# Kernel optimization log

Measured on AMD Instinct MI355X. Metric: run time of the kernel, lower is better.

Reference implementation:

```python
import jax, jax.numpy as jnp
import numpy as np

POS_INF = 64500.0
B, P, C = 32, 2048, 256
D = C // 2


def setup_inputs() -> dict:
    key = jax.random.key(0)
    ks = jax.random.split(key, 8)
    x = jax.random.normal(ks[0], (B, P, C), dtype=jnp.float32)
    mask = jax.random.randint(ks[1], (B, P), 0, 2).astype(jnp.float32)
    s = 0.05
    Wq = jax.random.normal(ks[2], (C, D), dtype=jnp.float32) * s
    bq = jnp.zeros((D,), dtype=jnp.float32)
    Wk = jax.random.normal(ks[3], (C, D), dtype=jnp.float32) * s
    bk = jnp.zeros((D,), dtype=jnp.float32)
    Wv = jax.random.normal(ks[4], (C, C), dtype=jnp.float32) * s
    bv = jnp.zeros((C,), dtype=jnp.float32)
    return {"x": x, "mask": mask, "Wq": Wq, "bq": bq, "Wk": Wk, "bk": bk, "Wv": Wv, "bv": bv}


def reference(x, mask, Wq, bq, Wk, bk, Wv, bv):
    # Projections (torch Linear: x @ W^T + b; weights here stored [in, out])
    q = x @ Wq + bq          # [B, P, D]
    k = x @ Wk + bk          # [B, P, D]
    v = x @ Wv + bv          # [B, P, C]
    scale = 1.0 / (D ** 0.5)
    attn = jnp.einsum('bpd,bqd->bpq', q, k) * scale   # [B, P, P]
    # additive mask bias broadcast over keys (masks query rows, as in source)
    bias = (mask[:, :, None] - 1.0) * POS_INF          # [B, P, 1]
    attn = jax.nn.softmax(attn + bias, axis=-1)
    out = jnp.einsum('bpq,bqc->bpc', attn, v)          # [B, P, C]
    return out * mask[:, :, None]
```

## Files before the change

kernel.cpp:

```cpp
#include <hip/hip_runtime.h>
#include <hip/hip_bf16.h>

typedef __attribute__((ext_vector_type(8))) short short8;
typedef __attribute__((ext_vector_type(4))) float f32x4;
typedef __attribute__((ext_vector_type(4))) unsigned int uint4v;
typedef unsigned int u32;
typedef __attribute__((address_space(3))) u32 lds_u32;
typedef const __attribute__((address_space(1))) u32 glb_u32;

#define NB 32
#define NP 2048
#define NC 256
#define ND 128

#define QSCALE (0.08838834764831845f * 1.4426950408889634f)
#define DEFER_THR 8.0f

__device__ inline float fast_exp2(float x){ return exp2f(x); }

__device__ inline unsigned short f2bf(float f){
  union { float f; unsigned u; } v; v.f = f;
  unsigned r = v.u + 0x7FFFu + ((v.u >> 16) & 1u);
  return (unsigned short)(r >> 16);
}
__device__ inline unsigned pk2(float a, float b){
  return (unsigned)f2bf(a) | ((unsigned)f2bf(b) << 16);
}
__device__ inline unsigned cvtpk(float a, float b){
  unsigned r;
  asm("v_cvt_pk_bf16_f32 %0, %1, %2" : "=v"(r) : "v"(a), "v"(b));
  return r;
}

__global__ __launch_bounds__(256) void prep_w(const float* __restrict__ Wq, const float* __restrict__ bq,
    const float* __restrict__ Wk, const float* __restrict__ bk,
    const float* __restrict__ Wv, const float* __restrict__ bv,
    unsigned short* __restrict__ WqkT, unsigned short* __restrict__ WvT, float* __restrict__ bqk){
  int o = blockIdx.x; int i = threadIdx.x;
  float wqk = (o < ND) ? Wq[i*ND + o] * QSCALE : Wk[i*ND + (o-ND)];
  WqkT[o*NC + i] = f2bf(wqk);
  WvT[o*NC + i]  = f2bf(Wv[i*NC + o]);
  if (i == 0) bqk[o] = (o < ND) ? bq[o]*QSCALE : bk[o-ND];
}

__global__ __launch_bounds__(256) void qkv_proj(const float* __restrict__ x,
    const unsigned short* __restrict__ WqkT, const float* __restrict__ bqk,
    const unsigned short* __restrict__ WvT, const float* __restrict__ bv,
    unsigned short* __restrict__ QK, unsigned short* __restrict__ VT){
  __shared__ unsigned short Alds[64*264];
  const int tid = threadIdx.x;
  const long rowbase = (long)blockIdx.x * 64;
  const int b = blockIdx.x >> 5, pt = blockIdx.x & 31;
  #pragma unroll
  for (int it = 0; it < 16; ++it){
    int chunk = tid + it*256;
    int r = chunk >> 6;
    int c4 = (chunk & 63) << 2;
    const float4 v = *(const float4*)(x + (rowbase + r)*NC + c4);
    *(uint2*)(&Alds[r*264 + c4]) = make_uint2(pk2(v.x, v.y), pk2(v.z, v.w));
  }
  __syncthreads();
  const int w = tid >> 6, lane = tid & 63, g = lane >> 4, c0 = lane & 15;
  const f32x4 zero = {0.f,0.f,0.f,0.f};

  {
    const int wrow = (w >> 1) * 32, wcol = (w & 1) * 128;
    f32x4 acc[2][8];
    #pragma unroll
    for (int m=0;m<2;m++){ for(int n=0;n<8;n++) acc[m][n] = zero; }
    #pragma unroll
    for (int ks=0; ks<8; ++ks){
      short8 a[2], bfr[8];
      #pragma unroll
      for (int m=0;m<2;m++)
        a[m] = *(const short8*)(&Alds[(wrow + 16*m + c0)*264 + ks*32 + 8*g]);
      #pragma unroll
      for (int n=0;n<8;n++)
        bfr[n] = *(const short8*)(&WqkT[(wcol + 16*n + c0)*NC + ks*32 + 8*g]);
      #pragma unroll
      for (int m=0;m<2;m++){
        #pragma unroll
        for(int n=0;n<8;n++)
          acc[m][n] = __builtin_amdgcn_mfma_f32_16x16x32_bf16(a[m], bfr[n], acc[m][n], 0,0,0);
      }
    }
    #pragma unroll
    for (int n=0;n<8;n++){
      int o = wcol + 16*n + c0;
      float bia = bqk[o];
      #pragma unroll
      for (int m=0;m<2;m++){
        long row = rowbase + wrow + 16*m + 4*g;
        #pragma unroll
        for (int r=0;r<4;r++)
          QK[(row + r)*NC + o] = f2bf(acc[m][n][r] + bia);
      }
    }
  }

  {
    const int wc = (w >> 1) * 128, wp = (w & 1) * 32;
    f32x4 acc[8][2];
    #pragma unroll
    for (int m=0;m<8;m++){ for(int n=0;n<2;n++) acc[m][n] = zero; }
    #pragma unroll
    for (int ks=0; ks<8; ++ks){
      short8 a[8], bb[2];
      #pragma unroll
      for (int m=0;m<8;m++)
        a[m] = *(const short8*)(&WvT[(wc + 16*m + c0)*NC + ks*32 + 8*g]);
      #pragma unroll
      for (int n=0;n<2;n++)
        bb[n] = *(const short8*)(&Alds[(wp + 16*n + c0)*264 + ks*32 + 8*g]);
      #pragma unroll
      for (int m=0;m<8;m++){
        #pragma unroll
        for(int n=0;n<2;n++)
          acc[m][n] = __builtin_amdgcn_mfma_f32_16x16x32_bf16(a[m], bb[n], acc[m][n], 0,0,0);
      }
    }
    #pragma unroll
    for (int m=0;m<8;m++){
      int cout = wc + 16*m + 4*g;
      #pragma unroll
      for (int r=0;r<4;r++){
        float bia = bv[cout + r];
        long base = ((long)b*NC + cout + r)*NP + pt*64 + wp;
        #pragma unroll
        for (int n=0;n<2;n++)
          VT[base + 16*n + c0] = f2bf(acc[m][n][r] + bia);
      }
    }
  }
}

__global__ __launch_bounds__(256,2) void attn(const unsigned short* __restrict__ QK,
    const unsigned short* __restrict__ VT, const float* __restrict__ mask,
    float* __restrict__ out){
  __shared__ unsigned short Klds[64*128];
  __shared__ unsigned short Vlds[256*64];
  const int tid = threadIdx.x;
  const int b = blockIdx.x >> 4, qt = blockIdx.x & 15;
  const int qbase = qt * 128;
  const int w = tid >> 6, lane = tid & 63, g = lane >> 4, c0 = lane & 15;
  const int c07 = (c0 & 7) << 3;
  unsigned short* pw = &Klds[w * 2048];

  const uint4v onesu = {0x3F803F80u, 0x3F803F80u, 0x3F803F80u, 0x3F803F80u};
  const short8 vones = __builtin_bit_cast(short8, onesu);

  const long qrow0 = (long)b * NP + qbase + w*32;
  short8 qf[2][4];
  #pragma unroll
  for (int n2=0;n2<2;n2++)
    #pragma unroll
    for (int ks=0; ks<4; ++ks)
      qf[n2][ks] = *(const short8*)(&QK[(qrow0 + n2*16 + c0)*NC + ks*32 + 8*g]);

  const f32x4 zero = {0.f,0.f,0.f,0.f};
  f32x4 oacc[2][16];
  f32x4 oacc_l[2];
  #pragma unroll
  for (int n2=0;n2<2;n2++){
    for (int n=0;n<16;n++) oacc[n2][n] = zero;
    oacc_l[n2] = zero;
  }
  float m_run[2] = {-1e30f, -1e30f};
  const long kvbase = (long)b * NP;
  const long vtbase = (long)b * NC * NP;

  for (int t=0; t<32; ++t){
    const int kb = t*64;
    __syncthreads();
    #pragma unroll
    for (int j=0;j<4;++j){
      int chunk = w*256 + j*64 + lane;
      int key = chunk >> 4, sp = chunk & 15;
      const unsigned short* src = &QK[(kvbase + kb + key)*NC + ND + ((sp ^ (key&7))*8)];
      __builtin_amdgcn_global_load_lds((glb_u32*)src, (lds_u32*)&Klds[(w*256 + j*64)*8], 16, 0, 0);
    }
    #pragma unroll
    for (int j=0;j<8;++j){
      int chunk = w*512 + j*64 + lane;
      int crow = chunk >> 3, sp = chunk & 7;
      const unsigned short* src = &VT[vtbase + (long)crow*NP + kb + ((sp ^ (crow&7))*8)];
      __builtin_amdgcn_global_load_lds((glb_u32*)src, (lds_u32*)&Vlds[(w*512 + j*64)*8], 16, 0, 0);
    }
    __syncthreads();

    f32x4 st[4][2];
    #pragma unroll
    for (int m=0;m<4;m++){ st[m][0] = zero; st[m][1] = zero; }
    __builtin_amdgcn_s_setprio(1);
    #pragma unroll
    for (int ks=0;ks<4;ks++){
      short8 ka[4];
      #pragma unroll
      for (int m=0;m<4;m++)
        ka[m] = *(const short8*)(&Klds[(16*m + c0)*128 + ((ks*32 + 8*g) ^ c07)]);
      #pragma unroll
      for (int m=0;m<4;m++){
        st[m][0] = __builtin_amdgcn_mfma_f32_16x16x32_bf16(ka[m], qf[0][ks], st[m][0], 0,0,0);
        st[m][1] = __builtin_amdgcn_mfma_f32_16x16x32_bf16(ka[m], qf[1][ks], st[m][1], 0,0,0);
      }
    }
    __builtin_amdgcn_s_setprio(0);

    #pragma unroll
    for (int n2=0;n2<2;n2++){
      float tm = st[0][n2][0];
      #pragma unroll
      for (int m=0;m<4;m++){
        #pragma unroll
        for (int r=0;r<4;r++) tm = fmaxf(tm, st[m][n2][r]);
      }
      tm = fmaxf(tm, __shfl_xor(tm, 16));
      tm = fmaxf(tm, __shfl_xor(tm, 32));
      if (!__all(tm <= m_run[n2] + DEFER_THR)){
        float mn = fmaxf(m_run[n2], tm);
        float alpha = fast_exp2(m_run[n2] - mn);
        m_run[n2] = mn;
        float ar[4];
        #pragma unroll
        for (int r=0;r<4;r++) ar[r] = __shfl(alpha, 4*g + r);
        #pragma unroll
        for (int n=0;n<16;n++){
          #pragma unroll
          for (int r=0;r<4;r++) oacc[n2][n][r] *= ar[r];
        }
        #pragma unroll
        for (int r=0;r<4;r++) oacc_l[n2][r] *= ar[r];
      }
      const float mr = m_run[n2];
      #pragma unroll
      for (int m=0;m<4;m++){
        #pragma unroll
        for (int r=0;r<4;r++)
          st[m][n2][r] = fast_exp2(st[m][n2][r] - mr);
      }
    }

    __syncthreads();

    #pragma unroll
    for (int n2=0;n2<2;n2++){
      const int prow = n2*16 + c0;
      const int pxor = (prow & 7) << 3;
      #pragma unroll
      for (int m=0;m<4;m++){
        uint2 pd;
        pd.x = cvtpk(st[m][n2][0], st[m][n2][1]);
        pd.y = cvtpk(st[m][n2][2], st[m][n2][3]);
        *(uint2*)(&pw[prow*64 + ((16*m + 4*g) ^ pxor)]) = pd;
      }
    }

    __builtin_amdgcn_s_setprio(1);
    #pragma unroll
    for (int kk=0;kk<2;kk++){
      short8 pa[2];
      pa[0] = *(const short8*)(&pw[(c0     )*64 + ((kk*32 + 8*g) ^ ((c0&7)<<3))]);
      pa[1] = *(const short8*)(&pw[(16 + c0)*64 + ((kk*32 + 8*g) ^ ((c0&7)<<3))]);
      oacc_l[0] = __builtin_amdgcn_mfma_f32_16x16x32_bf16(pa[0], vones, oacc_l[0], 0,0,0);
      oacc_l[1] = __builtin_amdgcn_mfma_f32_16x16x32_bf16(pa[1], vones, oacc_l[1], 0,0,0);
      #pragma unroll
      for (int n=0;n<16;n++){
        short8 vb = *(const short8*)(&Vlds[(16*n + c0)*64 + ((kk*32 + 8*g) ^ c07)]);
        oacc[0][n] = __builtin_amdgcn_mfma_f32_16x16x32_bf16(pa[0], vb, oacc[0][n], 0,0,0);
        oacc[1][n] = __builtin_amdgcn_mfma_f32_16x16x32_bf16(pa[1], vb, oacc[1][n], 0,0,0);
      }
    }
    __builtin_amdgcn_s_setprio(0);
  }

  #pragma unroll
  for (int n2=0;n2<2;n2++){
    float fac[4];
    #pragma unroll
    for (int r=0;r<4;r++){
      long q = qbase + w*32 + n2*16 + 4*g + r;
      fac[r] = mask[(long)b*NP + q] / oacc_l[n2][r];
    }
    #pragma unroll
    for (int n=0;n<16;n++){
      #pragma unroll
      for (int r=0;r<4;r++){
        long q = qbase + w*32 + n2*16 + 4*g + r;
        out[((long)b*NP + q)*NC + 16*n + c0] = oacc[n2][n][r] * fac[r];
      }
    }
  }
}

extern "C" void kernel_launch(void* const* d_in, const int* in_sizes, int n_in,
                              void* d_out, int out_size, void* d_ws, size_t ws_size,
                              hipStream_t stream){
  const float* x    = (const float*)d_in[0];
  const float* mask = (const float*)d_in[1];
  const float* Wq   = (const float*)d_in[2];
  const float* bq   = (const float*)d_in[3];
  const float* Wk   = (const float*)d_in[4];
  const float* bk   = (const float*)d_in[5];
  const float* Wv   = (const float*)d_in[6];
  const float* bv   = (const float*)d_in[7];
  float* outp = (float*)d_out;
  char* ws = (char*)d_ws;

  unsigned short* QK   = (unsigned short*)(ws);
  unsigned short* VT   = (unsigned short*)(ws + 33554432);
  char* scratch        = (char*)d_out;
  unsigned short* WqkT = (unsigned short*)(scratch);
  unsigned short* WvT  = (unsigned short*)(scratch + 131072);
  float* bqk           = (float*)(scratch + 262144);

  prep_w  <<<256, 256, 0, stream>>>(Wq, bq, Wk, bk, Wv, bv, WqkT, WvT, bqk);
  qkv_proj<<<1024, 256, 0, stream>>>(x, WqkT, bqk, WvT, bv, QK, VT);
  attn    <<<512, 256, 0, stream>>>(QK, VT, mask, outp);
}
```

Before: 219.3 us.

## Compact unmasked query rows and skip attention for masked queries

```diff
diff --git a/kernel.cpp b/kernel.cpp
--- a/kernel.cpp
+++ b/kernel.cpp
@@ -134,14 +134,51 @@
   }
 }
 
+__global__ __launch_bounds__(256) void build_idx(const float* __restrict__ mask,
+    int* __restrict__ qidx, int* __restrict__ cnt){
+  __shared__ int lsc[256];
+  const int b = blockIdx.x, tid = threadIdx.x;
+  const int base = tid * 8;
+  int loc[8]; int myc = 0;
+  #pragma unroll
+  for (int j=0;j<8;j++){
+    loc[j] = (mask[(long)b*NP + base + j] != 0.0f) ? 1 : 0;
+    myc += loc[j];
+  }
+  int sum = myc;
+  lsc[tid] = sum; __syncthreads();
+  for (int off=1; off<256; off<<=1){
+    int t = (tid >= off) ? lsc[tid-off] : 0;
+    __syncthreads();
+    sum += t; lsc[tid] = sum;
+    __syncthreads();
+  }
+  int start = sum - myc;
+  #pragma unroll
+  for (int j=0;j<8;j++){
+    if (loc[j]) qidx[(long)b*NP + (start++)] = base + j;
+  }
+  if (tid == 255) cnt[b] = sum;
+}
+
+__global__ __launch_bounds__(256) void zero_masked(const float* __restrict__ mask,
+    float4* __restrict__ out4){
+  const long i = (long)blockIdx.x * 256 + threadIdx.x;
+  const long row = i >> 6;
+  if (mask[row] == 0.0f) out4[i] = make_float4(0.f,0.f,0.f,0.f);
+}
+
 __global__ __launch_bounds__(256,2) void attn(const unsigned short* __restrict__ QK,
-    const unsigned short* __restrict__ VT, const float* __restrict__ mask,
-    float* __restrict__ out){
+    const unsigned short* __restrict__ VT, const int* __restrict__ qidx,
+    const int* __restrict__ cnt, float* __restrict__ out){
+  const int b = blockIdx.x >> 4, qt = blockIdx.x & 15;
+  const int count = cnt[b];
+  const int qbase = qt * 128;
+  if (qbase >= count) return;
+
   __shared__ unsigned short Klds[64*128];
   __shared__ unsigned short Vlds[256*64];
   const int tid = threadIdx.x;
-  const int b = blockIdx.x >> 4, qt = blockIdx.x & 15;
-  const int qbase = qt * 128;
   const int w = tid >> 6, lane = tid & 63, g = lane >> 4, c0 = lane & 15;
   const int c07 = (c0 & 7) << 3;
   unsigned short* pw = &Klds[w * 2048];
@@ -149,13 +186,19 @@
   const uint4v onesu = {0x3F803F80u, 0x3F803F80u, 0x3F803F80u, 0x3F803F80u};
   const short8 vones = __builtin_bit_cast(short8, onesu);
 
-  const long qrow0 = (long)b * NP + qbase + w*32;
+  int qrowA[2];
+  #pragma unroll
+  for (int n2=0;n2<2;n2++){
+    int slot = qbase + w*32 + n2*16 + c0;
+    slot = (slot < count) ? slot : (count - 1);
+    qrowA[n2] = qidx[(long)b*NP + slot];
+  }
   short8 qf[2][4];
   #pragma unroll
   for (int n2=0;n2<2;n2++)
     #pragma unroll
     for (int ks=0; ks<4; ++ks)
-      qf[n2][ks] = *(const short8*)(&QK[(qrow0 + n2*16 + c0)*NC + ks*32 + 8*g]);
+      qf[n2][ks] = *(const short8*)(&QK[((long)b*NP + qrowA[n2])*NC + ks*32 + 8*g]);
 
   const f32x4 zero = {0.f,0.f,0.f,0.f};
   f32x4 oacc[2][16];
@@ -275,19 +318,16 @@
 
   #pragma unroll
   for (int n2=0;n2<2;n2++){
-    float fac[4];
     #pragma unroll
     for (int r=0;r<4;r++){
-      long q = qbase + w*32 + n2*16 + 4*g + r;
-      fac[r] = mask[(long)b*NP + q] / oacc_l[n2][r];
-    }
-    #pragma unroll
-    for (int n=0;n<16;n++){
-      #pragma unroll
-      for (int r=0;r<4;r++){
-        long q = qbase + w*32 + n2*16 + 4*g + r;
-        out[((long)b*NP + q)*NC + 16*n + c0] = oacc[n2][n][r] * fac[r];
-      }
+      int slot = qbase + w*32 + n2*16 + 4*g + r;
+      slot = (slot < count) ? slot : (count - 1);
+      const int qrow = qidx[(long)b*NP + slot];
+      const float fac = 1.0f / oacc_l[n2][r];
+      float* orow = &out[((long)b*NP + qrow)*NC];
+      #pragma unroll
+      for (int n=0;n<16;n++)
+        orow[16*n + c0] = oacc[n2][n][r] * fac;
     }
   }
 }
@@ -308,12 +348,16 @@
 
   unsigned short* QK   = (unsigned short*)(ws);
   unsigned short* VT   = (unsigned short*)(ws + 33554432);
+  int* qidx            = (int*)(ws + 67108864);
+  int* cnt             = (int*)(ws + 67371008);
   char* scratch        = (char*)d_out;
   unsigned short* WqkT = (unsigned short*)(scratch);
   unsigned short* WvT  = (unsigned short*)(scratch + 131072);
   float* bqk           = (float*)(scratch + 262144);
 
-  prep_w  <<<256, 256, 0, stream>>>(Wq, bq, Wk, bk, Wv, bv, WqkT, WvT, bqk);
-  qkv_proj<<<1024, 256, 0, stream>>>(x, WqkT, bqk, WvT, bv, QK, VT);
-  attn    <<<512, 256, 0, stream>>>(QK, VT, mask, outp);
-}
+  prep_w     <<<256, 256, 0, stream>>>(Wq, bq, Wk, bk, Wv, bv, WqkT, WvT, bqk);
+  qkv_proj   <<<1024, 256, 0, stream>>>(x, WqkT, bqk, WvT, bv, QK, VT);
+  build_idx  <<<NB, 256, 0, stream>>>(mask, qidx, cnt);
+  zero_masked<<<16384, 256, 0, stream>>>(mask, (float4*)outp);
+  attn       <<<512, 256, 0, stream>>>(QK, VT, qidx, cnt, outp);
+}
```

After: 236.8 us. +8.0%, slower.
